# Kernel optimization log

Hardware: AMD Instinct MI355X
Metric: run time of the kernel (lower is better)

The kernel has to match this reference:

```python
import jax, jax.numpy as jnp
import numpy as np

N = 50000        # num_electrodes / nodes
C = 32           # in_channels
H = 32           # hid_channels
K = 3            # num Chebyshev layers
E = 1_600_000    # num edges (avg degree 32)
FC_HID = 64      # fc1 hidden size
NUM_CLASSES = 2
BN_EPS = 1e-5


def setup_inputs() -> dict:
    key = jax.random.key(0)
    ks = jax.random.split(key, 10)
    x = jax.random.normal(ks[0], (N, C), dtype=jnp.float32)
    edge_index = jax.random.randint(ks[1], (2, E), 0, N, dtype=jnp.int64)
    edge_weight = jax.random.uniform(ks[2], (E,), dtype=jnp.float32)
    # per-layer GraphConvolution weights [K, C, H] (xavier-ish scale)
    W = jax.random.normal(ks[3], (K, C, H), dtype=jnp.float32) * (2.0 / (C + H)) ** 0.5
    # BatchNorm1d(in_channels) parameters (eval mode, running stats)
    bn_gamma = jnp.ones((C,), dtype=jnp.float32)
    bn_beta = jnp.zeros((C,), dtype=jnp.float32)
    bn_mean = jax.random.normal(ks[4], (C,), dtype=jnp.float32) * 0.01
    bn_var = jax.random.uniform(ks[5], (C,), dtype=jnp.float32) * 0.5 + 0.5
    # fc1: Linear(N*H -> FC_HID), fc2: Linear(FC_HID -> NUM_CLASSES)
    fc1_w = jax.random.normal(ks[6], (FC_HID, N * H), dtype=jnp.float32) * 1e-3
    fc1_b = jnp.zeros((FC_HID,), dtype=jnp.float32)
    fc2_w = jax.random.normal(ks[7], (NUM_CLASSES, FC_HID), dtype=jnp.float32) * 0.1
    fc2_b = jnp.zeros((NUM_CLASSES,), dtype=jnp.float32)
    return {
        "x": x, "edge_weight": edge_weight, "W": W,
        "bn_gamma": bn_gamma, "bn_beta": bn_beta, "bn_mean": bn_mean, "bn_var": bn_var,
        "fc1_w": fc1_w, "fc1_b": fc1_b, "fc2_w": fc2_w, "fc2_b": fc2_b,
        "edge_index": edge_index,
    }


def reference(x, edge_weight, W, bn_gamma, bn_beta, bn_mean, bn_var,
              fc1_w, fc1_b, fc2_w, fc2_b, edge_index):
    # BatchNorm1d over channels (eval mode): x is [N, C]
    x = (x - bn_mean) * jax.lax.rsqrt(bn_var + BN_EPS) * bn_gamma + bn_beta

    src, dst = edge_index[0], edge_index[1]
    self_loop = (src == dst)
    xj = x[src]  # gather source node features [E, C]

    # k == 0 term: edge weights replaced by self-loop indicator (T_0 identity term)
    w0 = jnp.where(self_loop, jnp.float32(1.0), jnp.float32(0.0))
    agg0 = jax.ops.segment_sum(w0[:, None] * xj, dst, num_segments=N)      # [N, C]
    # k >= 1 terms all share the same aggregated message (same edge_weight),
    # so aggregate once and contract with the summed weights W[1:]
    agg = jax.ops.segment_sum(edge_weight[:, None] * xj, dst, num_segments=N)  # [N, C]

    result = agg0 @ W[0] + agg @ W[1:].sum(axis=0)  # [N, H]
    result = jax.nn.relu(result).reshape(1, -1)     # [1, N*H]

    h = jax.nn.relu(result @ fc1_w.T + fc1_b)       # [1, FC_HID]
    out = h @ fc2_w.T + fc2_b                       # [1, NUM_CLASSES]
    return out
```

## Files before the change

kernel.cpp:

```cpp
#include <hip/hip_runtime.h>

constexpr int N_NODES = 50000;
constexpr int E_EDGES = 1600000;
constexpr int NH      = N_NODES * 32;
constexpr float BN_EPS = 1e-5f;
constexpr int NPAD    = 50016;
constexpr int NBLK    = 625;

__global__ void zero_kernel(float4* __restrict__ p, int n4) {
    int i = blockIdx.x * blockDim.x + threadIdx.x;
    if (i < n4) p[i] = make_float4(0.f, 0.f, 0.f, 0.f);
}

__global__ void hist_kernel(const int* __restrict__ ei, int* __restrict__ counts) {
    int e = blockIdx.x * blockDim.x + threadIdx.x;
    if (e < E_EDGES) atomicAdd(&counts[ei[E_EDGES + e]], 1);
}

__device__ inline int block_excl_scan(int v, int* s) {
    int t = threadIdx.x;
    s[t] = v;
    __syncthreads();
    for (int d = 1; d < 256; d <<= 1) {
        int x = (t >= d) ? s[t - d] : 0;
        __syncthreads();
        s[t] += x;
        __syncthreads();
    }
    return s[t] - v;
}

__global__ void scan1_kernel(const int* __restrict__ counts, int* __restrict__ bsum) {
    int i = blockIdx.x * 256 + threadIdx.x;
    int v = (i < N_NODES) ? counts[i] : 0;
#pragma unroll
    for (int o = 32; o > 0; o >>= 1) v += __shfl_down(v, o);
    __shared__ int s[4];
    int wave = threadIdx.x >> 6, lane = threadIdx.x & 63;
    if (lane == 0) s[wave] = v;
    __syncthreads();
    if (threadIdx.x == 0) bsum[blockIdx.x] = s[0] + s[1] + s[2] + s[3];
}

__global__ void scan2_kernel(int* __restrict__ bsum) {
    __shared__ int s[256];
    int t = threadIdx.x;
    int v = (t < 196) ? bsum[t] : 0;
    int excl = block_excl_scan(v, s);
    if (t < 196) bsum[t] = excl;
}

__global__ void scan3_kernel(const int* __restrict__ counts, const int* __restrict__ bsum,
                             int* __restrict__ off, int* __restrict__ cursor) {
    __shared__ int s[256];
    int i = blockIdx.x * 256 + threadIdx.x;
    int v = (i < N_NODES) ? counts[i] : 0;
    int excl = block_excl_scan(v, s) + bsum[blockIdx.x];
    if (i < N_NODES) { off[i] = excl; cursor[i] = excl; }
    if (i == N_NODES - 1) off[N_NODES] = excl + v;
}

__global__ void place_kernel(const int* __restrict__ ei, const float* __restrict__ ew,
                             int* __restrict__ cursor, int2* __restrict__ ep) {
    int e = blockIdx.x * blockDim.x + threadIdx.x;
    if (e < E_EDGES) {
        int src = ei[e];
        int dst = ei[E_EDGES + e];
        int pos = atomicAdd(&cursor[dst], 1);
        ep[pos] = make_int2(src | ((src == dst) ? 0x80000000 : 0),
                            __float_as_int(ew[e]));
    }
}

__global__ void gather_kernel(const float* __restrict__ x,
                              const float* __restrict__ gamma,
                              const float* __restrict__ beta,
                              const float* __restrict__ mean,
                              const float* __restrict__ var,
                              const int*   __restrict__ off,
                              const int2*  __restrict__ ep,
                              const float* __restrict__ W,
                              float* __restrict__ rres) {
    __shared__ float s_w0[1024], s_wsum[1024];
    int tid = threadIdx.x;
    for (int idx = tid; idx < 1024; idx += 256) {
        s_w0[idx]   = W[idx];
        s_wsum[idx] = W[1024 + idx] + W[2048 + idx];
    }
    __syncthreads();

    int n     = blockIdx.x * 8 + (tid >> 5);
    int c     = tid & 31;
    int gbase = tid & 32;

    float sc = gamma[c] * rsqrtf(var[c] + BN_EPS);
    float sh = beta[c] - mean[c] * sc;

    int e0 = off[n];
    int nb = off[n + 1] - e0;
    const int2* e2 = ep + e0;
    float acc = 0.f, acc0 = 0.f;

    int base = 0;
    for (; base + 32 <= nb; base += 32) {
        int2 p = e2[base + c];
        int sw = p.x; float wv = __int_as_float(p.y);
#pragma unroll 8
        for (int j = 0; j < 32; j++) {
            int   swj = __shfl(sw, gbase + j);
            float wj  = __shfl(wv, gbase + j);
            float v   = fmaf(x[(swj & 0x7fffffff) * 32 + c], sc, sh);
            acc = fmaf(wj, v, acc);
            if (swj < 0) acc0 += v;
        }
    }
    int rem = nb - base;
    if (rem > 0) {
        int sw = 0; float wv = 0.f;
        if (c < rem) { int2 p = e2[base + c]; sw = p.x; wv = __int_as_float(p.y); }
        for (int j = 0; j < rem; j++) {
            int   swj = __shfl(sw, gbase + j);
            float wj  = __shfl(wv, gbase + j);
            float v   = fmaf(x[(swj & 0x7fffffff) * 32 + c], sc, sh);
            acc = fmaf(wj, v, acc);
            if (swj < 0) acc0 += v;
        }
    }
    float r = 0.f;
#pragma unroll
    for (int cc = 0; cc < 32; cc++) {
        float a  = __shfl(acc,  gbase + cc);
        float a0 = __shfl(acc0, gbase + cc);
        r = fmaf(a,  s_wsum[cc * 32 + c], r);
        r = fmaf(a0, s_w0  [cc * 32 + c], r);
    }
    rres[n * 32 + c] = fmaxf(r, 0.f);
}

constexpr int CHUNK = 2560;
__global__ void fc1_kernel(const float* __restrict__ r,
                           const float* __restrict__ w,
                           float* __restrict__ partial) {
    __shared__ float4 s_r[640];
    int tid = threadIdx.x;
    size_t ib = (size_t)blockIdx.x * CHUNK;
    const float4* r4 = (const float4*)(r + ib);
    for (int i = tid; i < 640; i += 256) s_r[i] = r4[i];
    __syncthreads();

    int wave = tid >> 6, lane = tid & 63;
    int jbase = wave * 16;
    float* pout = partial + blockIdx.x * 64;
    for (int jj = 0; jj < 16; jj += 2) {
        const float4* wa = (const float4*)(w + (size_t)(jbase + jj    ) * NH + ib);
        const float4* wb = (const float4*)(w + (size_t)(jbase + jj + 1) * NH + ib);
        float a0 = 0.f, a1 = 0.f;
#pragma unroll
        for (int k = 0; k < 10; k++) {
            float4 rv = s_r[lane + k * 64];
            float4 x0 = wa[lane + k * 64];
            float4 x1 = wb[lane + k * 64];
            a0 = fmaf(rv.x, x0.x, a0); a0 = fmaf(rv.y, x0.y, a0);
            a0 = fmaf(rv.z, x0.z, a0); a0 = fmaf(rv.w, x0.w, a0);
            a1 = fmaf(rv.x, x1.x, a1); a1 = fmaf(rv.y, x1.y, a1);
            a1 = fmaf(rv.z, x1.z, a1); a1 = fmaf(rv.w, x1.w, a1);
        }
#pragma unroll
        for (int o = 32; o > 0; o >>= 1) {
            a0 += __shfl_down(a0, o);
            a1 += __shfl_down(a1, o);
        }
        if (lane == 0) {
            pout[jbase + jj    ] = a0;
            pout[jbase + jj + 1] = a1;
        }
    }
}

__global__ void reduce_head_kernel(const float* __restrict__ partial,
                                   const float* __restrict__ fc1_b,
                                   const float* __restrict__ fc2_w,
                                   const float* __restrict__ fc2_b,
                                   float* __restrict__ out) {
    __shared__ float red[1024];
    int t = threadIdx.x;
    int j = t & 63, s = t >> 6;
    float a = 0.f;
    for (int b = s; b < NBLK; b += 16) a += partial[b * 64 + j];
    red[t] = a;
    __syncthreads();
    if (s == 0) {
        float h = fc1_b[j];
#pragma unroll
        for (int q = 0; q < 16; q++) h += red[q * 64 + j];
        h = fmaxf(h, 0.f);
#pragma unroll
        for (int k = 0; k < 2; k++) {
            float p = h * fc2_w[k * 64 + j];
#pragma unroll
            for (int o = 32; o > 0; o >>= 1) p += __shfl_down(p, o);
            if (j == 0) out[k] = p + fc2_b[k];
        }
    }
}

extern "C" void kernel_launch(void* const* d_in, const int* in_sizes, int n_in,
                              void* d_out, int out_size, void* d_ws, size_t ws_size,
                              hipStream_t stream) {
    const float* x     = (const float*)d_in[0];
    const float* ew    = (const float*)d_in[1];
    const float* W     = (const float*)d_in[2];
    const float* gamma = (const float*)d_in[3];
    const float* beta  = (const float*)d_in[4];
    const float* mean  = (const float*)d_in[5];
    const float* var   = (const float*)d_in[6];
    const float* fc1_w = (const float*)d_in[7];
    const float* fc1_b = (const float*)d_in[8];
    const float* fc2_w = (const float*)d_in[9];
    const float* fc2_b = (const float*)d_in[10];
    const int*   ei    = (const int*)d_in[11];
    float* out = (float*)d_out;

    float* partial = (float*)d_ws;
    int*   counts  = (int*)d_ws + 40000;
    int*   off     = (int*)d_ws + 40000 + NPAD;
    int*   cursor  = (int*)d_ws + 40000 + 2 * NPAD;
    int*   bsum    = (int*)d_ws + 40000 + 3 * NPAD;
    int2*  ep      = (int2*)(bsum + 256);
    float* rres    = (float*)(ep + E_EDGES);
    (void)ws_size; (void)in_sizes; (void)n_in; (void)out_size;

    {
        int n4 = NPAD / 4;
        zero_kernel<<<(n4 + 255) / 256, 256, 0, stream>>>((float4*)counts, n4);
    }
    hist_kernel <<<(E_EDGES + 255) / 256, 256, 0, stream>>>(ei, counts);
    scan1_kernel<<<196, 256, 0, stream>>>(counts, bsum);
    scan2_kernel<<<1,   256, 0, stream>>>(bsum);
    scan3_kernel<<<196, 256, 0, stream>>>(counts, bsum, off, cursor);
    place_kernel<<<(E_EDGES + 255) / 256, 256, 0, stream>>>(ei, ew, cursor, ep);
    gather_kernel<<<N_NODES / 8, 256, 0, stream>>>(x, gamma, beta, mean, var,
                                                   off, ep, W, rres);
    fc1_kernel <<<NBLK, 256, 0, stream>>>(rres, fc1_w, partial);
    reduce_head_kernel<<<1, 1024, 0, stream>>>(partial, fc1_b, fc2_w, fc2_b, out);
}
```

Baseline: 835.6 us.

## Fuse CSR build into one persistent kernel and fuse gather with fc1 and head

The histogram, three scan kernels and edge placement are merged into one 196-block persistent kernel that uses software grid barriers. The gather/aggregation is fused with the fc1 dot product, so the per-node result stays in shared memory instead of round-tripping through global memory. A last-block-done atomic counter performs the final reduction and fc2 head inside the same kernel. This removes several launches and the rres buffer traffic, but the grid barriers assume all 196 blocks of 1024 threads are co-resident, and fewer CSR threads may slow the atomic phases.

New measurement: 1.363 ms. +63.2%, slower.

```diff
diff --git a/kernel.cpp b/kernel.cpp
--- a/kernel.cpp
+++ b/kernel.cpp
@@ -4,24 +4,26 @@
 constexpr int E_EDGES = 1600000;
 constexpr int NH      = N_NODES * 32;
 constexpr float BN_EPS = 1e-5f;
-constexpr int NPAD    = 50016;
-constexpr int NBLK    = 625;
+constexpr int NPAD    = 50176;
+
+constexpr int CSR_BLOCKS  = 196;
+constexpr int CSR_THREADS = 1024;
+constexpr int CSR_TOTAL   = CSR_BLOCKS * CSR_THREADS;
+
+constexpr int GBLK   = 1250;
+constexpr int GNODES = 40;
+constexpr int GCHUNK = GNODES * 32;
 
 __global__ void zero_kernel(float4* __restrict__ p, int n4) {
     int i = blockIdx.x * blockDim.x + threadIdx.x;
     if (i < n4) p[i] = make_float4(0.f, 0.f, 0.f, 0.f);
 }
 
-__global__ void hist_kernel(const int* __restrict__ ei, int* __restrict__ counts) {
-    int e = blockIdx.x * blockDim.x + threadIdx.x;
-    if (e < E_EDGES) atomicAdd(&counts[ei[E_EDGES + e]], 1);
-}
-
 __device__ inline int block_excl_scan(int v, int* s) {
     int t = threadIdx.x;
     s[t] = v;
     __syncthreads();
-    for (int d = 1; d < 256; d <<= 1) {
+    for (int d = 1; d < CSR_THREADS; d <<= 1) {
         int x = (t >= d) ? s[t - d] : 0;
         __syncthreads();
         s[t] += x;
@@ -30,40 +32,52 @@
     return s[t] - v;
 }
 
-__global__ void scan1_kernel(const int* __restrict__ counts, int* __restrict__ bsum) {
-    int i = blockIdx.x * 256 + threadIdx.x;
-    int v = (i < N_NODES) ? counts[i] : 0;
-#pragma unroll
-    for (int o = 32; o > 0; o >>= 1) v += __shfl_down(v, o);
-    __shared__ int s[4];
-    int wave = threadIdx.x >> 6, lane = threadIdx.x & 63;
-    if (lane == 0) s[wave] = v;
-    __syncthreads();
-    if (threadIdx.x == 0) bsum[blockIdx.x] = s[0] + s[1] + s[2] + s[3];
-}
-
-__global__ void scan2_kernel(int* __restrict__ bsum) {
-    __shared__ int s[256];
-    int t = threadIdx.x;
-    int v = (t < 196) ? bsum[t] : 0;
+__device__ inline void grid_barrier(int* ctr, int target) {
+    __syncthreads();
+    if (threadIdx.x == 0) {
+        __threadfence();
+        __hip_atomic_fetch_add(ctr, 1, __ATOMIC_ACQ_REL, __HIP_MEMORY_SCOPE_AGENT);
+        while (__hip_atomic_load(ctr, __ATOMIC_ACQUIRE, __HIP_MEMORY_SCOPE_AGENT) < target) {
+            __builtin_amdgcn_s_sleep(1);
+        }
+    }
+    __syncthreads();
+    __threadfence();
+}
+
+__global__ __launch_bounds__(CSR_THREADS)
+void csr_kernel(const int* __restrict__ ei, const float* __restrict__ ew,
+                int* __restrict__ ctrl, int* __restrict__ counts,
+                int* __restrict__ off, int* __restrict__ cursor,
+                int* __restrict__ bsum, int2* __restrict__ ep) {
+    __shared__ int s[CSR_THREADS];
+    int tid = blockIdx.x * CSR_THREADS + threadIdx.x;
+
+    for (int e = tid; e < E_EDGES; e += CSR_TOTAL)
+        atomicAdd(&counts[ei[E_EDGES + e]], 1);
+    grid_barrier(&ctrl[0], CSR_BLOCKS);
+
+    int v = (tid < N_NODES) ? counts[tid] : 0;
     int excl = block_excl_scan(v, s);
-    if (t < 196) bsum[t] = excl;
-}
-
-__global__ void scan3_kernel(const int* __restrict__ counts, const int* __restrict__ bsum,
-                             int* __restrict__ off, int* __restrict__ cursor) {
-    __shared__ int s[256];
-    int i = blockIdx.x * 256 + threadIdx.x;
-    int v = (i < N_NODES) ? counts[i] : 0;
-    int excl = block_excl_scan(v, s) + bsum[blockIdx.x];
-    if (i < N_NODES) { off[i] = excl; cursor[i] = excl; }
-    if (i == N_NODES - 1) off[N_NODES] = excl + v;
-}
-
-__global__ void place_kernel(const int* __restrict__ ei, const float* __restrict__ ew,
-                             int* __restrict__ cursor, int2* __restrict__ ep) {
-    int e = blockIdx.x * blockDim.x + threadIdx.x;
-    if (e < E_EDGES) {
+    if (threadIdx.x == CSR_THREADS - 1) bsum[blockIdx.x] = excl + v;
+    grid_barrier(&ctrl[1], CSR_BLOCKS);
+
+    int bv = (threadIdx.x < CSR_BLOCKS) ? bsum[threadIdx.x] : 0;
+    int bexcl = block_excl_scan(bv, s);
+    __syncthreads();
+    s[threadIdx.x] = bexcl;
+    __syncthreads();
+    int blockoff = s[blockIdx.x];
+
+    if (tid < N_NODES) {
+        int o = blockoff + excl;
+        off[tid] = o;
+        cursor[tid] = o;
+    }
+    if (tid == N_NODES - 1) off[N_NODES] = blockoff + excl + v;
+    grid_barrier(&ctrl[2], CSR_BLOCKS);
+
+    for (int e = tid; e < E_EDGES; e += CSR_TOTAL) {
         int src = ei[e];
         int dst = ei[E_EDGES + e];
         int pos = atomicAdd(&cursor[dst], 1);
@@ -72,16 +86,26 @@
     }
 }
 
-__global__ void gather_kernel(const float* __restrict__ x,
-                              const float* __restrict__ gamma,
-                              const float* __restrict__ beta,
-                              const float* __restrict__ mean,
-                              const float* __restrict__ var,
-                              const int*   __restrict__ off,
-                              const int2*  __restrict__ ep,
-                              const float* __restrict__ W,
-                              float* __restrict__ rres) {
-    __shared__ float s_w0[1024], s_wsum[1024];
+__global__ void gfc_kernel(const float* __restrict__ x,
+                           const float* __restrict__ gamma,
+                           const float* __restrict__ beta,
+                           const float* __restrict__ mean,
+                           const float* __restrict__ var,
+                           const int*   __restrict__ off,
+                           const int2*  __restrict__ ep,
+                           const float* __restrict__ W,
+                           const float* __restrict__ fc1_w,
+                           const float* __restrict__ fc1_b,
+                           const float* __restrict__ fc2_w,
+                           const float* __restrict__ fc2_b,
+                           float* __restrict__ partial,
+                           int*   __restrict__ ctrl,
+                           float* __restrict__ out) {
+    __shared__ float  s_w0[1024], s_wsum[1024];
+    __shared__ float4 s_r4[GCHUNK / 4];
+    __shared__ int    s_last;
+    float* s_r = (float*)s_r4;
+
     int tid = threadIdx.x;
     for (int idx = tid; idx < 1024; idx += 256) {
         s_w0[idx]   = W[idx];
@@ -89,75 +113,67 @@
     }
     __syncthreads();
 
-    int n     = blockIdx.x * 8 + (tid >> 5);
     int c     = tid & 31;
     int gbase = tid & 32;
-
     float sc = gamma[c] * rsqrtf(var[c] + BN_EPS);
     float sh = beta[c] - mean[c] * sc;
-
-    int e0 = off[n];
-    int nb = off[n + 1] - e0;
-    const int2* e2 = ep + e0;
-    float acc = 0.f, acc0 = 0.f;
-
-    int base = 0;
-    for (; base + 32 <= nb; base += 32) {
-        int2 p = e2[base + c];
-        int sw = p.x; float wv = __int_as_float(p.y);
+    int n0 = blockIdx.x * GNODES;
+
+    for (int r = tid >> 5; r < GNODES; r += 8) {
+        int n  = n0 + r;
+        int e0 = off[n];
+        int nb = off[n + 1] - e0;
+        const int2* e2 = ep + e0;
+        float acc = 0.f, acc0 = 0.f;
+
+        int base = 0;
+        for (; base + 32 <= nb; base += 32) {
+            int2 p = e2[base + c];
+            int sw = p.x; float wv = __int_as_float(p.y);
 #pragma unroll 8
-        for (int j = 0; j < 32; j++) {
-            int   swj = __shfl(sw, gbase + j);
-            float wj  = __shfl(wv, gbase + j);
-            float v   = fmaf(x[(swj & 0x7fffffff) * 32 + c], sc, sh);
-            acc = fmaf(wj, v, acc);
-            if (swj < 0) acc0 += v;
-        }
-    }
-    int rem = nb - base;
-    if (rem > 0) {
-        int sw = 0; float wv = 0.f;
-        if (c < rem) { int2 p = e2[base + c]; sw = p.x; wv = __int_as_float(p.y); }
-        for (int j = 0; j < rem; j++) {
-            int   swj = __shfl(sw, gbase + j);
-            float wj  = __shfl(wv, gbase + j);
-            float v   = fmaf(x[(swj & 0x7fffffff) * 32 + c], sc, sh);
-            acc = fmaf(wj, v, acc);
-            if (swj < 0) acc0 += v;
-        }
-    }
-    float r = 0.f;
-#pragma unroll
-    for (int cc = 0; cc < 32; cc++) {
-        float a  = __shfl(acc,  gbase + cc);
-        float a0 = __shfl(acc0, gbase + cc);
-        r = fmaf(a,  s_wsum[cc * 32 + c], r);
-        r = fmaf(a0, s_w0  [cc * 32 + c], r);
-    }
-    rres[n * 32 + c] = fmaxf(r, 0.f);
-}
-
-constexpr int CHUNK = 2560;
-__global__ void fc1_kernel(const float* __restrict__ r,
-                           const float* __restrict__ w,
-                           float* __restrict__ partial) {
-    __shared__ float4 s_r[640];
-    int tid = threadIdx.x;
-    size_t ib = (size_t)blockIdx.x * CHUNK;
-    const float4* r4 = (const float4*)(r + ib);
-    for (int i = tid; i < 640; i += 256) s_r[i] = r4[i];
+            for (int j = 0; j < 32; j++) {
+                int   swj = __shfl(sw, gbase + j);
+                float wj  = __shfl(wv, gbase + j);
+                float vv  = fmaf(x[(swj & 0x7fffffff) * 32 + c], sc, sh);
+                acc = fmaf(wj, vv, acc);
+                if (swj < 0) acc0 += vv;
+            }
+        }
+        int rem = nb - base;
+        if (rem > 0) {
+            int sw = 0; float wv = 0.f;
+            if (c < rem) { int2 p = e2[base + c]; sw = p.x; wv = __int_as_float(p.y); }
+            for (int j = 0; j < rem; j++) {
+                int   swj = __shfl(sw, gbase + j);
+                float wj  = __shfl(wv, gbase + j);
+                float vv  = fmaf(x[(swj & 0x7fffffff) * 32 + c], sc, sh);
+                acc = fmaf(wj, vv, acc);
+                if (swj < 0) acc0 += vv;
+            }
+        }
+        float rr = 0.f;
+#pragma unroll
+        for (int cc = 0; cc < 32; cc++) {
+            float a  = __shfl(acc,  gbase + cc);
+            float a0 = __shfl(acc0, gbase + cc);
+            rr = fmaf(a,  s_wsum[cc * 32 + c], rr);
+            rr = fmaf(a0, s_w0  [cc * 32 + c], rr);
+        }
+        s_r[r * 32 + c] = fmaxf(rr, 0.f);
+    }
     __syncthreads();
 
     int wave = tid >> 6, lane = tid & 63;
-    int jbase = wave * 16;
+    size_t ib = (size_t)blockIdx.x * GCHUNK;
     float* pout = partial + blockIdx.x * 64;
     for (int jj = 0; jj < 16; jj += 2) {
-        const float4* wa = (const float4*)(w + (size_t)(jbase + jj    ) * NH + ib);
-        const float4* wb = (const float4*)(w + (size_t)(jbase + jj + 1) * NH + ib);
+        int j0 = wave * 16 + jj;
+        const float4* wa = (const float4*)(fc1_w + (size_t)j0       * NH + ib);
+        const float4* wb = (const float4*)(fc1_w + (size_t)(j0 + 1) * NH + ib);
         float a0 = 0.f, a1 = 0.f;
 #pragma unroll
-        for (int k = 0; k < 10; k++) {
-            float4 rv = s_r[lane + k * 64];
+        for (int k = 0; k < GCHUNK / 256; k++) {
+            float4 rv = s_r4[lane + k * 64];
             float4 x0 = wa[lane + k * 64];
             float4 x1 = wb[lane + k * 64];
             a0 = fmaf(rv.x, x0.x, a0); a0 = fmaf(rv.y, x0.y, a0);
@@ -171,35 +187,38 @@
             a1 += __shfl_down(a1, o);
         }
         if (lane == 0) {
-            pout[jbase + jj    ] = a0;
-            pout[jbase + jj + 1] = a1;
-        }
-    }
-}
-
-__global__ void reduce_head_kernel(const float* __restrict__ partial,
-                                   const float* __restrict__ fc1_b,
-                                   const float* __restrict__ fc2_w,
-                                   const float* __restrict__ fc2_b,
-                                   float* __restrict__ out) {
-    __shared__ float red[1024];
-    int t = threadIdx.x;
-    int j = t & 63, s = t >> 6;
-    float a = 0.f;
-    for (int b = s; b < NBLK; b += 16) a += partial[b * 64 + j];
-    red[t] = a;
-    __syncthreads();
-    if (s == 0) {
-        float h = fc1_b[j];
-#pragma unroll
-        for (int q = 0; q < 16; q++) h += red[q * 64 + j];
-        h = fmaxf(h, 0.f);
-#pragma unroll
-        for (int k = 0; k < 2; k++) {
-            float p = h * fc2_w[k * 64 + j];
-#pragma unroll
-            for (int o = 32; o > 0; o >>= 1) p += __shfl_down(p, o);
-            if (j == 0) out[k] = p + fc2_b[k];
+            pout[j0]     = a0;
+            pout[j0 + 1] = a1;
+        }
+    }
+
+    __threadfence();
+    __syncthreads();
+    if (tid == 0) {
+        int prev = __hip_atomic_fetch_add(&ctrl[3], 1, __ATOMIC_ACQ_REL,
+                                          __HIP_MEMORY_SCOPE_AGENT);
+        s_last = (prev == GBLK - 1);
+    }
+    __syncthreads();
+    if (s_last) {
+        __threadfence();
+        float* red = s_w0;
+        int j = tid & 63, sl = tid >> 6;
+        float a = 0.f;
+#pragma unroll 4
+        for (int b = sl; b < GBLK; b += 4) a += partial[b * 64 + j];
+        red[tid] = a;
+        __syncthreads();
+        if (sl == 0) {
+            float h = fc1_b[j] + red[j] + red[j + 64] + red[j + 128] + red[j + 192];
+            h = fmaxf(h, 0.f);
+#pragma unroll
+            for (int k = 0; k < 2; k++) {
+                float p = h * fc2_w[k * 64 + j];
+#pragma unroll
+                for (int o = 32; o > 0; o >>= 1) p += __shfl_down(p, o);
+                if (j == 0) out[k] = p + fc2_b[k];
+            }
         }
     }
 }
@@ -221,26 +240,22 @@
     const int*   ei    = (const int*)d_in[11];
     float* out = (float*)d_out;
 
-    float* partial = (float*)d_ws;
-    int*   counts  = (int*)d_ws + 40000;
-    int*   off     = (int*)d_ws + 40000 + NPAD;
-    int*   cursor  = (int*)d_ws + 40000 + 2 * NPAD;
-    int*   bsum    = (int*)d_ws + 40000 + 3 * NPAD;
-    int2*  ep      = (int2*)(bsum + 256);
-    float* rres    = (float*)(ep + E_EDGES);
+    int*   ctrl    = (int*)d_ws;
+    int*   counts  = ctrl + 16;
+    int*   off     = counts + NPAD;
+    int*   cursor  = off + NPAD;
+    int*   bsum    = cursor + NPAD;
+    float* partial = (float*)(bsum + 256);
+    int2*  ep      = (int2*)(partial + GBLK * 64);
     (void)ws_size; (void)in_sizes; (void)n_in; (void)out_size;
 
     {
-        int n4 = NPAD / 4;
-        zero_kernel<<<(n4 + 255) / 256, 256, 0, stream>>>((float4*)counts, n4);
-    }
-    hist_kernel <<<(E_EDGES + 255) / 256, 256, 0, stream>>>(ei, counts);
-    scan1_kernel<<<196, 256, 0, stream>>>(counts, bsum);
-    scan2_kernel<<<1,   256, 0, stream>>>(bsum);
-    scan3_kernel<<<196, 256, 0, stream>>>(counts, bsum, off, cursor);
-    place_kernel<<<(E_EDGES + 255) / 256, 256, 0, stream>>>(ei, ew, cursor, ep);
-    gather_kernel<<<N_NODES / 8, 256, 0, stream>>>(x, gamma, beta, mean, var,
-                                                   off, ep, W, rres);
-    fc1_kernel <<<NBLK, 256, 0, stream>>>(rres, fc1_w, partial);
-    reduce_head_kernel<<<1, 1024, 0, stream>>>(partial, fc1_b, fc2_w, fc2_b, out);
-}
+        int n4 = (16 + NPAD) / 4;
+        zero_kernel<<<(n4 + 255) / 256, 256, 0, stream>>>((float4*)d_ws, n4);
+    }
+    csr_kernel<<<CSR_BLOCKS, CSR_THREADS, 0, stream>>>(ei, ew, ctrl, counts,
+                                                       off, cursor, bsum, ep);
+    gfc_kernel<<<GBLK, 256, 0, stream>>>(x, gamma, beta, mean, var, off, ep, W,
+                                         fc1_w, fc1_b, fc2_w, fc2_b,
+                                         partial, ctrl, out);
+}
```

## Split each node's edges across wave halves and batch two nodes per wave

Applied to the files above, without the earlier changes.

The gather kernel now gives each 64-lane wave two nodes in sequence. The two 32-lane halves process alternating edges of a node, so each edge pair is loaded directly rather than broadcast by shuffles, and the halves' partial sums are combined with an xor shuffle. The final 32x64 weight contraction goes through LDS with packed float2 weights, split across the two halves, instead of 64 shuffles per lane. This targets shuffle overhead and lane imbalance, at the cost of LDS traffic and wave barriers between nodes.

After: 816.2 us. 2.3% less time.

```diff
diff --git a/kernel.cpp b/kernel.cpp
--- a/kernel.cpp
+++ b/kernel.cpp
@@ -81,60 +81,77 @@
                               const int2*  __restrict__ ep,
                               const float* __restrict__ W,
                               float* __restrict__ rres) {
-    __shared__ float s_w0[1024], s_wsum[1024];
+    __shared__ float2 s_wp[1024];
+    __shared__ float  s_ap[4][64];
     int tid = threadIdx.x;
-    for (int idx = tid; idx < 1024; idx += 256) {
-        s_w0[idx]   = W[idx];
-        s_wsum[idx] = W[1024 + idx] + W[2048 + idx];
-    }
-    __syncthreads();
-
-    int n     = blockIdx.x * 8 + (tid >> 5);
-    int c     = tid & 31;
-    int gbase = tid & 32;
+    for (int idx = tid; idx < 1024; idx += 256)
+        s_wp[idx] = make_float2(W[1024 + idx] + W[2048 + idx], W[idx]);
+    __syncthreads();
+
+    int lane  = tid & 63;
+    int c     = lane & 31;
+    int half  = lane >> 5;
+    int wslot = tid >> 6;
+    int wid   = (blockIdx.x << 2) + wslot;
 
     float sc = gamma[c] * rsqrtf(var[c] + BN_EPS);
     float sh = beta[c] - mean[c] * sc;
 
-    int e0 = off[n];
-    int nb = off[n + 1] - e0;
-    const int2* e2 = ep + e0;
-    float acc = 0.f, acc0 = 0.f;
-
-    int base = 0;
-    for (; base + 32 <= nb; base += 32) {
-        int2 p = e2[base + c];
-        int sw = p.x; float wv = __int_as_float(p.y);
-#pragma unroll 8
-        for (int j = 0; j < 32; j++) {
-            int   swj = __shfl(sw, gbase + j);
-            float wj  = __shfl(wv, gbase + j);
-            float v   = fmaf(x[(swj & 0x7fffffff) * 32 + c], sc, sh);
-            acc = fmaf(wj, v, acc);
-            if (swj < 0) acc0 += v;
-        }
-    }
-    int rem = nb - base;
-    if (rem > 0) {
-        int sw = 0; float wv = 0.f;
-        if (c < rem) { int2 p = e2[base + c]; sw = p.x; wv = __int_as_float(p.y); }
-        for (int j = 0; j < rem; j++) {
-            int   swj = __shfl(sw, gbase + j);
-            float wj  = __shfl(wv, gbase + j);
-            float v   = fmaf(x[(swj & 0x7fffffff) * 32 + c], sc, sh);
-            acc = fmaf(wj, v, acc);
-            if (swj < 0) acc0 += v;
-        }
-    }
-    float r = 0.f;
-#pragma unroll
-    for (int cc = 0; cc < 32; cc++) {
-        float a  = __shfl(acc,  gbase + cc);
-        float a0 = __shfl(acc0, gbase + cc);
-        r = fmaf(a,  s_wsum[cc * 32 + c], r);
-        r = fmaf(a0, s_w0  [cc * 32 + c], r);
-    }
-    rres[n * 32 + c] = fmaxf(r, 0.f);
+    const float2* ap2 = (const float2*)s_ap[wslot];
+
+#pragma unroll
+    for (int i = 0; i < 2; i++) {
+        int n  = (wid << 1) + i;
+        int e0 = off[n];
+        int nb = off[n + 1] - e0;
+        const int2* e2 = ep + e0;
+
+        float acc = 0.f, acc0 = 0.f;
+        int base = 0;
+        for (; base + 8 <= nb; base += 8) {
+#pragma unroll
+            for (int k = 0; k < 4; k++) {
+                int2 p = e2[base + (k << 1) + half];
+                float vv = fmaf(x[(p.x & 0x7fffffff) * 32 + c], sc, sh);
+                acc = fmaf(__int_as_float(p.y), vv, acc);
+                if (p.x < 0) acc0 += vv;
+            }
+        }
+        for (; base + 2 <= nb; base += 2) {
+            int2 p = e2[base + half];
+            float vv = fmaf(x[(p.x & 0x7fffffff) * 32 + c], sc, sh);
+            acc = fmaf(__int_as_float(p.y), vv, acc);
+            if (p.x < 0) acc0 += vv;
+        }
+        if (base < nb && half == 0) {
+            int2 p = e2[base];
+            float vv = fmaf(x[(p.x & 0x7fffffff) * 32 + c], sc, sh);
+            acc = fmaf(__int_as_float(p.y), vv, acc);
+            if (p.x < 0) acc0 += vv;
+        }
+
+        acc  += __shfl_xor(acc,  32);
+        acc0 += __shfl_xor(acc0, 32);
+
+        __builtin_amdgcn_wave_barrier();
+        s_ap[wslot][(c << 1) | half] = half ? acc0 : acc;
+        __threadfence_block();
+        __builtin_amdgcn_wave_barrier();
+
+        float r = 0.f;
+        int ccb = half << 4;
+#pragma unroll
+        for (int t = 0; t < 16; t++) {
+            int cc = ccb + t;
+            float2 ap = ap2[cc];
+            float2 wp = s_wp[cc * 32 + c];
+            r = fmaf(ap.x, wp.x, r);
+            r = fmaf(ap.y, wp.y, r);
+        }
+        r += __shfl_xor(r, 32);
+        if (half == 0) rres[n * 32 + c] = fmaxf(r, 0.f);
+        __builtin_amdgcn_wave_barrier();
+    }
 }
 
 constexpr int CHUNK = 2560;
```
